# Optimization experiments

Measured on AMD Instinct MI355X. Metric: run time of the kernel, lower is better.

Reference implementation:

```python
import jax, jax.numpy as jnp
import numpy as np

D = 1024
K = 3  # depthwise conv kernel size, causal (left pad K-1)


def setup_inputs() -> dict:
    key = jax.random.key(0)
    ks = jax.random.split(key, 6)
    B, L = 16, 2048
    x = jax.random.normal(ks[0], (B, L, D), dtype=jnp.float32)
    s_in = 1.0 / np.sqrt(D)
    Win = jax.random.uniform(ks[1], (3 * D, D), minval=-s_in, maxval=s_in, dtype=jnp.float32)
    bin_ = jax.random.uniform(ks[2], (3 * D,), minval=-s_in, maxval=s_in, dtype=jnp.float32)
    # depthwise Conv1d weight (D, 1, K) -> stored as (D, K)
    s_c = 1.0 / np.sqrt(K)  # fan_in = in_channels/groups * K = K
    wconv = jax.random.uniform(ks[3], (D, K), minval=-s_c, maxval=s_c, dtype=jnp.float32)
    Wout = jax.random.uniform(ks[4], (D, D), minval=-s_in, maxval=s_in, dtype=jnp.float32)
    bout = jax.random.uniform(ks[5], (D,), minval=-s_in, maxval=s_in, dtype=jnp.float32)
    return {"x": x, "Win": Win, "bin_": bin_, "wconv": wconv, "Wout": Wout, "bout": bout}


def reference(x, Win, bin_, wconv, Wout, bout):
    # x: (B, L, D). in_proj -> (B, L, 3D); chunk along channel dim == last dim here
    BCx = jnp.einsum('bld,ed->ble', x, Win) + bin_
    Bg, Cg, xg = jnp.split(BCx, 3, axis=-1)  # each (B, L, D)
    Bx = Bg * xg
    L = Bx.shape[1]
    # causal depthwise conv: pad K-1 zeros on the left of time axis
    xp = jnp.pad(Bx, ((0, 0), (K - 1, 0), (0, 0)))
    conv_out = (wconv[:, 0] * xp[:, 0:L]
                + wconv[:, 1] * xp[:, 1:L + 1]
                + wconv[:, 2] * xp[:, 2:L + 2])  # (B, L, D)
    y = Cg * conv_out
    return jnp.einsum('bld,ed->ble', y, Wout) + bout
```

## Files before the change

kernel.cpp:

```cpp
#include <hip/hip_runtime.h>
#include <hip/hip_bf16.h>

#define D_    1024
#define LSEQ  2048
#define M_    32768
#define K_    1024

typedef __bf16 bf16x8 __attribute__((ext_vector_type(8)));
typedef float  f32x4  __attribute__((ext_vector_type(4)));

__device__ __forceinline__ unsigned short f2bf(float f) {
  unsigned u = __float_as_uint(f);
  u += 0x7FFFu + ((u >> 16) & 1u);
  return (unsigned short)(u >> 16);
}
__device__ __forceinline__ float bf2f(unsigned short h) {
  return __uint_as_float(((unsigned)h) << 16);
}

__global__ __launch_bounds__(256) void cvt_f32_bf16(const float* __restrict__ in,
                                                    unsigned short* __restrict__ out,
                                                    int n4) {
  int i = blockIdx.x * 256 + threadIdx.x;
  if (i < n4) {
    float4 v = ((const float4*)in)[i];
    ushort4 o;
    o.x = f2bf(v.x); o.y = f2bf(v.y); o.z = f2bf(v.z); o.w = f2bf(v.w);
    ((ushort4*)out)[i] = o;
  }
}

#define BK 32

__device__ __forceinline__ void gload_lds16(const void* g, void* l) {
  __builtin_amdgcn_global_load_lds((const __attribute__((address_space(1))) void*)g,
                                   (__attribute__((address_space(3))) void*)l,
                                   16, 0, 0);
}

template <int MODE>
__global__ __launch_bounds__(256) void gemm_fused(const unsigned short* __restrict__ A,
                                                  const unsigned short* __restrict__ Wb,
                                                  const float* __restrict__ biasA,
                                                  const float* __restrict__ biasB,
                                                  const unsigned short* __restrict__ Bx,
                                                  const float* __restrict__ wconv,
                                                  void* __restrict__ Outv) {
  __shared__ __align__(16) char smem[16896];
  unsigned short* As = (unsigned short*)smem;
  unsigned short* Bs = (unsigned short*)(smem + 8192);
  float* tr = (float*)smem;

  const int tid  = threadIdx.x;
  const int lane = tid & 63;
  const int wave = tid >> 6;
  const int quad = lane >> 4;
  const int l16  = lane & 15;
  const int wm   = wave & 1;
  const int wn   = wave >> 1;
  const int m0   = blockIdx.y * 128;

  const unsigned short* B0p;
  const unsigned short* B1p;
  int n0;
  if (MODE == 0) {
    n0  = blockIdx.x * 64;
    B0p = Wb + (long)n0 * K_;
    B1p = Wb + (long)(2048 + n0) * K_;
  } else if (MODE == 1) {
    n0  = blockIdx.x * 128;
    B0p = Wb + (long)(1024 + n0) * K_;
    B1p = B0p + (long)64 * K_;
  } else {
    n0  = blockIdx.x * 128;
    B0p = Wb + (long)n0 * K_;
    B1p = B0p + (long)64 * K_;
  }

  const int r0 = tid >> 2;
  const int s0 = (tid & 3) * 8;
  const unsigned short* a0 = A + (long)(m0 + r0) * K_ + s0;
  const unsigned short* a1 = a0 + (long)64 * K_;
  const unsigned short* b0 = B0p + (long)r0 * K_ + s0;
  const unsigned short* b1 = B1p + (long)r0 * K_ + s0;
  unsigned short* lA0 = &As[tid * 8];
  unsigned short* lA1 = &As[(256 + tid) * 8];
  unsigned short* lB0 = &Bs[tid * 8];
  unsigned short* lB1 = &Bs[(256 + tid) * 8];

  f32x4 acc[4][4] = {};

  for (int k0 = 0; k0 < K_; k0 += BK) {
    gload_lds16(a0 + k0, lA0);
    gload_lds16(a1 + k0, lA1);
    gload_lds16(b0 + k0, lB0);
    gload_lds16(b1 + k0, lB1);
    __syncthreads();

    bf16x8 af[4], bfr[4];
#pragma unroll
    for (int mi = 0; mi < 4; ++mi)
      af[mi] = *(const bf16x8*)&As[(wm * 64 + mi * 16 + l16) * BK + quad * 8];
#pragma unroll
    for (int ni = 0; ni < 4; ++ni)
      bfr[ni] = *(const bf16x8*)&Bs[(wn * 64 + ni * 16 + l16) * BK + quad * 8];

#pragma unroll
    for (int mi = 0; mi < 4; ++mi)
#pragma unroll
      for (int ni = 0; ni < 4; ++ni)
        acc[mi][ni] = __builtin_amdgcn_mfma_f32_16x16x32_bf16(af[mi], bfr[ni],
                                                              acc[mi][ni], 0, 0, 0);
    __syncthreads();
  }

  float bv[4];
#pragma unroll
  for (int ni = 0; ni < 4; ++ni) {
    int col = wn * 64 + ni * 16 + l16;
    if (MODE == 0)
      bv[ni] = (col < 64) ? biasA[n0 + col] : biasB[n0 + col - 64];
    else
      bv[ni] = biasA[n0 + col];
  }

  const int rr   = tid >> 3;
  const int cgid = tid & 7;

#pragma unroll
  for (int mi = 0; mi < 4; ++mi) {
#pragma unroll
    for (int ni = 0; ni < 4; ++ni) {
      int col = wn * 64 + ni * 16 + l16;
      f32x4 v = acc[mi][ni];
#pragma unroll
      for (int r = 0; r < 4; ++r)
        tr[(wm * 16 + quad * 4 + r) * 132 + col] = v[r] + bv[ni];
    }
    __syncthreads();

    int grow = m0 + (rr >> 4) * 64 + mi * 16 + (rr & 15);

    if (MODE == 0) {
      unsigned short* Out = (unsigned short*)Outv;
#pragma unroll
      for (int j = 0; j < 2; ++j) {
        int c = (cgid + j * 8) * 4;
        f32x4 bg = *(const f32x4*)&tr[rr * 132 + c];
        f32x4 xg = *(const f32x4*)&tr[rr * 132 + 64 + c];
        ushort4 o;
        o.x = f2bf(bg[0] * xg[0]); o.y = f2bf(bg[1] * xg[1]);
        o.z = f2bf(bg[2] * xg[2]); o.w = f2bf(bg[3] * xg[3]);
        *(ushort4*)&Out[(long)grow * D_ + n0 + c] = o;
      }
    } else if (MODE == 1) {
      unsigned short* Y = (unsigned short*)Outv;
      int l = grow & (LSEQ - 1);
#pragma unroll
      for (int j = 0; j < 4; ++j) {
        int c = (cgid + j * 8) * 4;
        int d = n0 + c;
        f32x4 cg = *(const f32x4*)&tr[rr * 132 + c];
        f32x4 w0 = *(const f32x4*)&wconv[d * 3];
        f32x4 w1 = *(const f32x4*)&wconv[d * 3 + 4];
        f32x4 w2 = *(const f32x4*)&wconv[d * 3 + 8];
        float wk0[4] = {w0[0], w0[3], w1[2], w2[1]};
        float wk1[4] = {w0[1], w1[0], w1[3], w2[2]};
        float wk2[4] = {w0[2], w1[1], w2[0], w2[3]};
        ushort4 zz = {0, 0, 0, 0};
        ushort4 x0 = *(const ushort4*)&Bx[(long)grow * D_ + d];
        ushort4 x1 = (l >= 1) ? *(const ushort4*)&Bx[(long)(grow - 1) * D_ + d] : zz;
        ushort4 x2 = (l >= 2) ? *(const ushort4*)&Bx[(long)(grow - 2) * D_ + d] : zz;
        ushort4 o;
        o.x = f2bf(cg[0] * (wk0[0] * bf2f(x2.x) + wk1[0] * bf2f(x1.x) + wk2[0] * bf2f(x0.x)));
        o.y = f2bf(cg[1] * (wk0[1] * bf2f(x2.y) + wk1[1] * bf2f(x1.y) + wk2[1] * bf2f(x0.y)));
        o.z = f2bf(cg[2] * (wk0[2] * bf2f(x2.z) + wk1[2] * bf2f(x1.z) + wk2[2] * bf2f(x0.z)));
        o.w = f2bf(cg[3] * (wk0[3] * bf2f(x2.w) + wk1[3] * bf2f(x1.w) + wk2[3] * bf2f(x0.w)));
        *(ushort4*)&Y[(long)grow * D_ + d] = o;
      }
    } else {
      float* Out = (float*)Outv;
#pragma unroll
      for (int j = 0; j < 4; ++j) {
        int c = (cgid + j * 8) * 4;
        f32x4 v = *(const f32x4*)&tr[rr * 132 + c];
        *(f32x4*)&Out[(long)grow * D_ + n0 + c] = v;
      }
    }
    __syncthreads();
  }
}

extern "C" void kernel_launch(void* const* d_in, const int* in_sizes, int n_in,
                              void* d_out, int out_size, void* d_ws, size_t ws_size,
                              hipStream_t stream) {
  const float* x     = (const float*)d_in[0];
  const float* Win   = (const float*)d_in[1];
  const float* bin   = (const float*)d_in[2];
  const float* wconv = (const float*)d_in[3];
  const float* Wout  = (const float*)d_in[4];
  const float* bout  = (const float*)d_in[5];

  char* ws = (char*)d_ws;
  unsigned short* x_b    = (unsigned short*)(ws);
  unsigned short* Win_b  = (unsigned short*)(ws + 67108864);
  unsigned short* Wout_b = (unsigned short*)(ws + 73400320);
  unsigned short* Bx_b   = (unsigned short*)(ws + 75497472);
  unsigned short* y_b    = (unsigned short*)(ws + 142606336);

  cvt_f32_bf16<<<(M_ * K_ / 4) / 256, 256, 0, stream>>>(x, x_b, M_ * K_ / 4);
  cvt_f32_bf16<<<(3072 * K_ / 4) / 256, 256, 0, stream>>>(Win, Win_b, 3072 * K_ / 4);
  cvt_f32_bf16<<<(D_ * K_ / 4) / 256, 256, 0, stream>>>(Wout, Wout_b, D_ * K_ / 4);

  {
    dim3 grid(D_ / 64, M_ / 128);
    gemm_fused<0><<<grid, 256, 0, stream>>>(x_b, Win_b, bin, bin + 2048,
                                            nullptr, nullptr, Bx_b);
  }
  {
    dim3 grid(D_ / 128, M_ / 128);
    gemm_fused<1><<<grid, 256, 0, stream>>>(x_b, Win_b, bin + 1024, nullptr,
                                            Bx_b, wconv, y_b);
  }
  {
    dim3 grid(D_ / 128, M_ / 128);
    gemm_fused<2><<<grid, 256, 0, stream>>>(y_b, Wout_b, bout, nullptr,
                                            nullptr, nullptr, d_out);
  }
}
```

Measured before the change: 631.4 us.

## Merge in-projection GEMMs with XCD-aware tile mapping and split out conv kernel

The two in-projection GEMM launches become one launch, and a 1D grid maps blocks so that tiles sharing the same rows of x land on the same XCD, improving L2 reuse of A. The depthwise conv and gating move out of the GEMM epilogue into a separate elementwise kernel that reads Bx and Cg (now stored to workspace as bf16). The three conversion kernels are merged into one launch, and the output GEMM also gets the XCD-aware tile swizzle. The cost is an extra write and read of the Cg intermediate in exchange for fewer launches and better cache locality.

```diff
diff --git a/kernel.cpp b/kernel.cpp
--- a/kernel.cpp
+++ b/kernel.cpp
@@ -5,6 +5,7 @@
 #define LSEQ  2048
 #define M_    32768
 #define K_    1024
+#define BK    32
 
 typedef __bf16 bf16x8 __attribute__((ext_vector_type(8)));
 typedef float  f32x4  __attribute__((ext_vector_type(4)));
@@ -18,38 +19,50 @@
   return __uint_as_float(((unsigned)h) << 16);
 }
 
-__global__ __launch_bounds__(256) void cvt_f32_bf16(const float* __restrict__ in,
-                                                    unsigned short* __restrict__ out,
-                                                    int n4) {
-  int i = blockIdx.x * 256 + threadIdx.x;
-  if (i < n4) {
-    float4 v = ((const float4*)in)[i];
-    ushort4 o;
-    o.x = f2bf(v.x); o.y = f2bf(v.y); o.z = f2bf(v.z); o.w = f2bf(v.w);
-    ((ushort4*)out)[i] = o;
-  }
-}
-
-#define BK 32
-
 __device__ __forceinline__ void gload_lds16(const void* g, void* l) {
   __builtin_amdgcn_global_load_lds((const __attribute__((address_space(1))) void*)g,
                                    (__attribute__((address_space(3))) void*)l,
                                    16, 0, 0);
 }
 
-template <int MODE>
-__global__ __launch_bounds__(256) void gemm_fused(const unsigned short* __restrict__ A,
-                                                  const unsigned short* __restrict__ Wb,
-                                                  const float* __restrict__ biasA,
-                                                  const float* __restrict__ biasB,
-                                                  const unsigned short* __restrict__ Bx,
-                                                  const float* __restrict__ wconv,
-                                                  void* __restrict__ Outv) {
+#define NX4  (M_ * K_ / 4)
+#define NW4  (3072 * K_ / 4)
+#define NO4  (D_ * K_ / 4)
+__global__ __launch_bounds__(256) void cvt_all(const float* __restrict__ x,
+                                               const float* __restrict__ Win,
+                                               const float* __restrict__ Wout,
+                                               unsigned short* __restrict__ x_b,
+                                               unsigned short* __restrict__ Win_b,
+                                               unsigned short* __restrict__ Wout_b) {
+  int i = blockIdx.x * 256 + threadIdx.x;
+  const float* src;
+  unsigned short* dst;
+  int off;
+  if (i < NX4)            { src = x;    dst = x_b;    off = i; }
+  else if (i < NX4 + NW4) { src = Win;  dst = Win_b;  off = i - NX4; }
+  else                    { src = Wout; dst = Wout_b; off = i - NX4 - NW4; }
+  float4 v = ((const float4*)src)[off];
+  ushort4 o;
+  o.x = f2bf(v.x); o.y = f2bf(v.y); o.z = f2bf(v.z); o.w = f2bf(v.w);
+  ((ushort4*)dst)[off] = o;
+}
+
+__global__ __launch_bounds__(256) void gemm_inproj(const unsigned short* __restrict__ A,
+                                                   const unsigned short* __restrict__ Wb,
+                                                   const float* __restrict__ bin,
+                                                   unsigned short* __restrict__ Bx,
+                                                   unsigned short* __restrict__ Cg) {
   __shared__ __align__(16) char smem[16896];
   unsigned short* As = (unsigned short*)smem;
   unsigned short* Bs = (unsigned short*)(smem + 8192);
   float* tr = (float*)smem;
+
+  const int g   = blockIdx.x;
+  const int xcd = g & 7;
+  const int u   = g >> 3;
+  const int m0  = (xcd + 8 * (u / 24)) * 128;
+  const int c   = u % 24;
+  const int paired = (c < 16);
 
   const int tid  = threadIdx.x;
   const int lane = tid & 63;
@@ -58,22 +71,17 @@
   const int l16  = lane & 15;
   const int wm   = wave & 1;
   const int wn   = wave >> 1;
-  const int m0   = blockIdx.y * 128;
-
+
+  int n0;
   const unsigned short* B0p;
   const unsigned short* B1p;
-  int n0;
-  if (MODE == 0) {
-    n0  = blockIdx.x * 64;
+  if (paired) {
+    n0  = c * 64;
     B0p = Wb + (long)n0 * K_;
     B1p = Wb + (long)(2048 + n0) * K_;
-  } else if (MODE == 1) {
-    n0  = blockIdx.x * 128;
+  } else {
+    n0  = (c - 16) * 128;
     B0p = Wb + (long)(1024 + n0) * K_;
-    B1p = B0p + (long)64 * K_;
-  } else {
-    n0  = blockIdx.x * 128;
-    B0p = Wb + (long)n0 * K_;
     B1p = B0p + (long)64 * K_;
   }
 
@@ -118,10 +126,10 @@
 #pragma unroll
   for (int ni = 0; ni < 4; ++ni) {
     int col = wn * 64 + ni * 16 + l16;
-    if (MODE == 0)
-      bv[ni] = (col < 64) ? biasA[n0 + col] : biasB[n0 + col - 64];
+    if (paired)
+      bv[ni] = (col < 64) ? bin[n0 + col] : bin[2048 + n0 + col - 64];
     else
-      bv[ni] = biasA[n0 + col];
+      bv[ni] = bin[1024 + n0 + col];
   }
 
   const int rr   = tid >> 3;
@@ -141,51 +149,150 @@
 
     int grow = m0 + (rr >> 4) * 64 + mi * 16 + (rr & 15);
 
-    if (MODE == 0) {
-      unsigned short* Out = (unsigned short*)Outv;
+    if (paired) {
 #pragma unroll
       for (int j = 0; j < 2; ++j) {
-        int c = (cgid + j * 8) * 4;
-        f32x4 bg = *(const f32x4*)&tr[rr * 132 + c];
-        f32x4 xg = *(const f32x4*)&tr[rr * 132 + 64 + c];
+        int cc = (cgid + j * 8) * 4;
+        f32x4 bg = *(const f32x4*)&tr[rr * 132 + cc];
+        f32x4 xg = *(const f32x4*)&tr[rr * 132 + 64 + cc];
         ushort4 o;
         o.x = f2bf(bg[0] * xg[0]); o.y = f2bf(bg[1] * xg[1]);
         o.z = f2bf(bg[2] * xg[2]); o.w = f2bf(bg[3] * xg[3]);
-        *(ushort4*)&Out[(long)grow * D_ + n0 + c] = o;
-      }
-    } else if (MODE == 1) {
-      unsigned short* Y = (unsigned short*)Outv;
-      int l = grow & (LSEQ - 1);
-#pragma unroll
-      for (int j = 0; j < 4; ++j) {
-        int c = (cgid + j * 8) * 4;
-        int d = n0 + c;
-        f32x4 cg = *(const f32x4*)&tr[rr * 132 + c];
-        f32x4 w0 = *(const f32x4*)&wconv[d * 3];
-        f32x4 w1 = *(const f32x4*)&wconv[d * 3 + 4];
-        f32x4 w2 = *(const f32x4*)&wconv[d * 3 + 8];
-        float wk0[4] = {w0[0], w0[3], w1[2], w2[1]};
-        float wk1[4] = {w0[1], w1[0], w1[3], w2[2]};
-        float wk2[4] = {w0[2], w1[1], w2[0], w2[3]};
-        ushort4 zz = {0, 0, 0, 0};
-        ushort4 x0 = *(const ushort4*)&Bx[(long)grow * D_ + d];
-        ushort4 x1 = (l >= 1) ? *(const ushort4*)&Bx[(long)(grow - 1) * D_ + d] : zz;
-        ushort4 x2 = (l >= 2) ? *(const ushort4*)&Bx[(long)(grow - 2) * D_ + d] : zz;
-        ushort4 o;
-        o.x = f2bf(cg[0] * (wk0[0] * bf2f(x2.x) + wk1[0] * bf2f(x1.x) + wk2[0] * bf2f(x0.x)));
-        o.y = f2bf(cg[1] * (wk0[1] * bf2f(x2.y) + wk1[1] * bf2f(x1.y) + wk2[1] * bf2f(x0.y)));
-        o.z = f2bf(cg[2] * (wk0[2] * bf2f(x2.z) + wk1[2] * bf2f(x1.z) + wk2[2] * bf2f(x0.z)));
-        o.w = f2bf(cg[3] * (wk0[3] * bf2f(x2.w) + wk1[3] * bf2f(x1.w) + wk2[3] * bf2f(x0.w)));
-        *(ushort4*)&Y[(long)grow * D_ + d] = o;
+        *(ushort4*)&Bx[(long)grow * D_ + n0 + cc] = o;
       }
     } else {
-      float* Out = (float*)Outv;
 #pragma unroll
       for (int j = 0; j < 4; ++j) {
-        int c = (cgid + j * 8) * 4;
-        f32x4 v = *(const f32x4*)&tr[rr * 132 + c];
-        *(f32x4*)&Out[(long)grow * D_ + n0 + c] = v;
+        int cc = (cgid + j * 8) * 4;
+        f32x4 v = *(const f32x4*)&tr[rr * 132 + cc];
+        ushort4 o;
+        o.x = f2bf(v[0]); o.y = f2bf(v[1]); o.z = f2bf(v[2]); o.w = f2bf(v[3]);
+        *(ushort4*)&Cg[(long)grow * D_ + n0 + cc] = o;
       }
+    }
+    __syncthreads();
+  }
+}
+
+__global__ __launch_bounds__(256) void conv_mul(const unsigned short* __restrict__ Bx,
+                                                const unsigned short* __restrict__ Cg,
+                                                const float* __restrict__ wconv,
+                                                unsigned short* __restrict__ y) {
+  __shared__ float wt[3][D_];
+  for (int i = threadIdx.x; i < D_; i += 256) {
+    wt[0][i] = wconv[i * 3 + 0];
+    wt[1][i] = wconv[i * 3 + 1];
+    wt[2][i] = wconv[i * 3 + 2];
+  }
+  __syncthreads();
+
+  int idx = blockIdx.x * 256 + threadIdx.x;
+  int bl  = idx >> 7;
+  int d8  = (idx & 127) * 8;
+  int l   = bl & (LSEQ - 1);
+
+  typedef unsigned short us8 __attribute__((ext_vector_type(8)));
+  us8 zz = {0, 0, 0, 0, 0, 0, 0, 0};
+  us8 x0 = *(const us8*)&Bx[(long)bl * D_ + d8];
+  us8 x1 = (l >= 1) ? *(const us8*)&Bx[(long)(bl - 1) * D_ + d8] : zz;
+  us8 x2 = (l >= 2) ? *(const us8*)&Bx[(long)(bl - 2) * D_ + d8] : zz;
+  us8 cg = *(const us8*)&Cg[(long)bl * D_ + d8];
+
+  us8 o;
+#pragma unroll
+  for (int j = 0; j < 8; ++j) {
+    float conv = wt[0][d8 + j] * bf2f(x2[j]) + wt[1][d8 + j] * bf2f(x1[j])
+               + wt[2][d8 + j] * bf2f(x0[j]);
+    o[j] = f2bf(bf2f(cg[j]) * conv);
+  }
+  *(us8*)&y[(long)bl * D_ + d8] = o;
+}
+
+__global__ __launch_bounds__(256) void gemm_out(const unsigned short* __restrict__ A,
+                                                const unsigned short* __restrict__ Wb,
+                                                const float* __restrict__ bias,
+                                                float* __restrict__ Out) {
+  __shared__ __align__(16) char smem[16896];
+  unsigned short* As = (unsigned short*)smem;
+  unsigned short* Bs = (unsigned short*)(smem + 8192);
+  float* tr = (float*)smem;
+
+  const int g   = blockIdx.x;
+  const int u   = g >> 3;
+  const int m0  = ((g & 7) + 8 * (u >> 3)) * 128;
+  const int n0  = (u & 7) * 128;
+
+  const int tid  = threadIdx.x;
+  const int lane = tid & 63;
+  const int wave = tid >> 6;
+  const int quad = lane >> 4;
+  const int l16  = lane & 15;
+  const int wm   = wave & 1;
+  const int wn   = wave >> 1;
+
+  const int r0 = tid >> 2;
+  const int s0 = (tid & 3) * 8;
+  const unsigned short* a0 = A + (long)(m0 + r0) * K_ + s0;
+  const unsigned short* a1 = a0 + (long)64 * K_;
+  const unsigned short* b0 = Wb + (long)(n0 + r0) * K_ + s0;
+  const unsigned short* b1 = b0 + (long)64 * K_;
+  unsigned short* lA0 = &As[tid * 8];
+  unsigned short* lA1 = &As[(256 + tid) * 8];
+  unsigned short* lB0 = &Bs[tid * 8];
+  unsigned short* lB1 = &Bs[(256 + tid) * 8];
+
+  f32x4 acc[4][4] = {};
+
+  for (int k0 = 0; k0 < K_; k0 += BK) {
+    gload_lds16(a0 + k0, lA0);
+    gload_lds16(a1 + k0, lA1);
+    gload_lds16(b0 + k0, lB0);
+    gload_lds16(b1 + k0, lB1);
+    __syncthreads();
+
+    bf16x8 af[4], bfr[4];
+#pragma unroll
+    for (int mi = 0; mi < 4; ++mi)
+      af[mi] = *(const bf16x8*)&As[(wm * 64 + mi * 16 + l16) * BK + quad * 8];
+#pragma unroll
+    for (int ni = 0; ni < 4; ++ni)
+      bfr[ni] = *(const bf16x8*)&Bs[(wn * 64 + ni * 16 + l16) * BK + quad * 8];
+
+#pragma unroll
+    for (int mi = 0; mi < 4; ++mi)
+#pragma unroll
+      for (int ni = 0; ni < 4; ++ni)
+        acc[mi][ni] = __builtin_amdgcn_mfma_f32_16x16x32_bf16(af[mi], bfr[ni],
+                                                              acc[mi][ni], 0, 0, 0);
+    __syncthreads();
+  }
+
+  float bv[4];
+#pragma unroll
+  for (int ni = 0; ni < 4; ++ni)
+    bv[ni] = bias[n0 + wn * 64 + ni * 16 + l16];
+
+  const int rr   = tid >> 3;
+  const int cgid = tid & 7;
+
+#pragma unroll
+  for (int mi = 0; mi < 4; ++mi) {
+#pragma unroll
+    for (int ni = 0; ni < 4; ++ni) {
+      int col = wn * 64 + ni * 16 + l16;
+      f32x4 v = acc[mi][ni];
+#pragma unroll
+      for (int r = 0; r < 4; ++r)
+        tr[(wm * 16 + quad * 4 + r) * 132 + col] = v[r] + bv[ni];
+    }
+    __syncthreads();
+
+    int grow = m0 + (rr >> 4) * 64 + mi * 16 + (rr & 15);
+#pragma unroll
+    for (int j = 0; j < 4; ++j) {
+      int cc = (cgid + j * 8) * 4;
+      f32x4 v = *(const f32x4*)&tr[rr * 132 + cc];
+      *(f32x4*)&Out[(long)grow * D_ + n0 + cc] = v;
     }
     __syncthreads();
   }
@@ -206,25 +313,14 @@
   unsigned short* Win_b  = (unsigned short*)(ws + 67108864);
   unsigned short* Wout_b = (unsigned short*)(ws + 73400320);
   unsigned short* Bx_b   = (unsigned short*)(ws + 75497472);
-  unsigned short* y_b    = (unsigned short*)(ws + 142606336);
-
-  cvt_f32_bf16<<<(M_ * K_ / 4) / 256, 256, 0, stream>>>(x, x_b, M_ * K_ / 4);
-  cvt_f32_bf16<<<(3072 * K_ / 4) / 256, 256, 0, stream>>>(Win, Win_b, 3072 * K_ / 4);
-  cvt_f32_bf16<<<(D_ * K_ / 4) / 256, 256, 0, stream>>>(Wout, Wout_b, D_ * K_ / 4);
-
-  {
-    dim3 grid(D_ / 64, M_ / 128);
-    gemm_fused<0><<<grid, 256, 0, stream>>>(x_b, Win_b, bin, bin + 2048,
-                                            nullptr, nullptr, Bx_b);
-  }
-  {
-    dim3 grid(D_ / 128, M_ / 128);
-    gemm_fused<1><<<grid, 256, 0, stream>>>(x_b, Win_b, bin + 1024, nullptr,
-                                            Bx_b, wconv, y_b);
-  }
-  {
-    dim3 grid(D_ / 128, M_ / 128);
-    gemm_fused<2><<<grid, 256, 0, stream>>>(y_b, Wout_b, bout, nullptr,
-                                            nullptr, nullptr, d_out);
-  }
-}
+  unsigned short* Cg_b   = (unsigned short*)(ws + 142606336);
+  unsigned short* y_b    = (unsigned short*)(ws + 209715200);
+
+  cvt_all<<<(NX4 + NW4 + NO4) / 256, 256, 0, stream>>>(x, Win, Wout, x_b, Win_b, Wout_b);
+
+  gemm_inproj<<<6144, 256, 0, stream>>>(x_b, Win_b, bin, Bx_b, Cg_b);
+
+  conv_mul<<<(M_ * (D_ / 8)) / 256, 256, 0, stream>>>(Bx_b, Cg_b, wconv, y_b);
+
+  gemm_out<<<2048, 256, 0, stream>>>(y_b, Wout_b, bout, (float*)d_out);
+}
```

Result: faster. 594.3 us (-5.9%).
